# Kernel optimization log

Measured on AMD Instinct MI355X. Metric: run time of the kernel, lower is better.

Reference implementation:

```python
import jax, jax.numpy as jnp
import numpy as np

B, N, S, K = 8, 16384, 1024, 32
C_STEM, C_PATCH, PE_DIM = 64, 128, 24
RADIUS = 0.2
NUM_BANDS = PE_DIM // 6  # 4 freq bands, sin+cos per xyz axis -> 3*2*4 = 24


def setup_inputs() -> dict:
    key = jax.random.key(0)
    ks = jax.random.split(key, 6)
    xyz = jax.random.uniform(ks[0], (B, N, 3), dtype=jnp.float32)
    point_feature = jax.random.normal(ks[1], (B, N, C_STEM), dtype=jnp.float32)
    patch_center = jax.random.uniform(ks[2], (B, S, 3), dtype=jnp.float32)
    in_dim = C_STEM + 3 + PE_DIM  # grouped_feature + relative_xyz + pos-enc
    w1 = jax.random.normal(ks[3], (in_dim, C_PATCH), dtype=jnp.float32) / np.sqrt(in_dim)
    b1 = jnp.zeros((C_PATCH,), dtype=jnp.float32)
    w2 = jax.random.normal(ks[4], (C_PATCH, C_PATCH), dtype=jnp.float32) / np.sqrt(C_PATCH)
    b2 = jnp.zeros((C_PATCH,), dtype=jnp.float32)
    return dict(xyz=xyz, point_feature=point_feature, patch_center=patch_center,
                w1=w1, b1=b1, w2=w2, b2=b2)


def query_ball_point(radius, nsample, xyz, new_xyz):
    # Standard PointNet++ ball query. xyz:[B,N,3], new_xyz:[B,S,3] -> idx:[B,S,K]
    n = xyz.shape[1]
    sqrdists = jnp.sum((new_xyz[:, :, None, :] - xyz[:, None, :, :]) ** 2, axis=-1)  # [B,S,N]
    gi = jnp.where(sqrdists > radius * radius, n,
                   jnp.arange(n, dtype=jnp.int32)[None, None, :])
    gi = jnp.sort(gi, axis=-1)[:, :, :nsample]           # first K in-ball indices
    first = gi[:, :, :1]
    gi = jnp.where(gi == n, first, gi)                   # pad misses with first hit
    return jnp.minimum(gi, n - 1)


def index_points(points, idx):
    # points:[B,N,C], idx:[B,S,K] -> [B,S,K,C]
    b = points.shape[0]
    return points[jnp.arange(b)[:, None, None], idx]


def pos_encode(rel):
    # NeRF-style sinusoidal encoding of relative xyz: [...,3] -> [...,PE_DIM]
    freqs = (2.0 ** jnp.arange(NUM_BANDS, dtype=jnp.float32)) * jnp.pi
    ang = rel[..., None] * freqs                          # [...,3,NB]
    enc = jnp.concatenate([jnp.sin(ang), jnp.cos(ang)], axis=-1)  # [...,3,2NB]
    return enc.reshape(rel.shape[:-1] + (PE_DIM,))


def reference(xyz, point_feature, patch_center, w1, b1, w2, b2):
    neighbor_idx = query_ball_point(RADIUS, K, xyz, patch_center)   # [B,S,K]
    grouped_xyz = index_points(xyz, neighbor_idx)                    # [B,S,K,3]
    grouped_feature = index_points(point_feature, neighbor_idx)      # [B,S,K,C_STEM]
    relative_xyz = grouped_xyz - patch_center[:, :, None, :]
    relative_position = pos_encode(relative_xyz)                     # [B,S,K,PE_DIM]
    grouped_input = jnp.concatenate(
        (grouped_feature, relative_xyz, relative_position), axis=-1)  # [B,S,K,91]
    h = jax.nn.relu(grouped_input @ w1 + b1)   # PointMLP 1 (shared per-point MLP)
    h = h @ w2 + b2                            # PointMLP 2 (no activation)
    patch_feature = jnp.max(h, axis=2)         # max-pool over K neighbors -> [B,S,C_PATCH]
    return (patch_feature, neighbor_idx)
```

## Files before the change

kernel.cpp:

```cpp
#include <hip/hip_runtime.h>
#include <hip/hip_bf16.h>

#define B_ 8
#define N_ 16384
#define S_ 1024
#define K_ 32
#define CSTEM 64
#define CPATCH 128
#define INDIM 91
#define LDH 136

typedef __attribute__((ext_vector_type(8))) short short8v;
typedef __attribute__((ext_vector_type(4))) float f32x4;

static __device__ __forceinline__ unsigned short f2bf(float f) {
  union { float f; unsigned int u; } v; v.f = f;
  return (unsigned short)((v.u + 0x7FFFu + ((v.u >> 16) & 1u)) >> 16);
}

static __device__ __forceinline__ short8v cvt8(const float4 a, const float4 b) {
  unsigned short v[8];
  v[0] = f2bf(a.x); v[1] = f2bf(a.y); v[2] = f2bf(a.z); v[3] = f2bf(a.w);
  v[4] = f2bf(b.x); v[5] = f2bf(b.y); v[6] = f2bf(b.z); v[7] = f2bf(b.w);
  return *(const short8v*)v;
}

static __device__ __forceinline__ short8v pe_frag(
    float r0, float r1, float r2, int kq)
{
  unsigned short v[8];
  #pragma unroll
  for (int j = 0; j < 8; ++j) {
    const int c = 64 + kq + j;
    float val;
    if (c < 67) {
      val = (c == 64) ? r0 : ((c == 65) ? r1 : r2);
    } else if (c < 91) {
      const int qq = c - 67, d = qq >> 3, rbit = qq & 7, band = rbit & 3;
      const float rel = (d == 0) ? r0 : ((d == 1) ? r1 : r2);
      const float ang = rel * ((float)(1 << band) * 3.14159265358979323846f);
      val = (rbit < 4) ? __sinf(ang) : __cosf(ang);
    } else {
      val = 0.f;
    }
    v[j] = f2bf(val);
  }
  return *(const short8v*)v;
}

__global__ __launch_bounds__(256) void pack_weights(
    const float* __restrict__ w1, const float* __restrict__ w2,
    unsigned short* __restrict__ w1p, unsigned short* __restrict__ w2p)
{
  const int id = blockIdx.x * 256 + threadIdx.x;
  if (id < 3 * 8 * 64) {
    const int l = id & 63, ct = (id >> 6) & 7, ks = id >> 9;
    const int col = 16 * ct + (l & 15);
    const int kb = 32 * ks + (l >> 4) * 8;
    unsigned short v[8];
    #pragma unroll
    for (int j = 0; j < 8; ++j) {
      const int k = kb + j;
      v[j] = (k < INDIM) ? f2bf(w1[k * CPATCH + col]) : (unsigned short)0;
    }
    *(short8v*)&w1p[(size_t)id * 8] = *(const short8v*)v;
  } else if (id < 3 * 8 * 64 + 4 * 8 * 64) {
    const int id2 = id - 3 * 8 * 64;
    const int l = id2 & 63, ct = (id2 >> 6) & 7, ks = id2 >> 9;
    const int col = 16 * ct + (l & 15);
    const int kb = 32 * ks + (l >> 4) * 8;
    unsigned short v[8];
    #pragma unroll
    for (int j = 0; j < 8; ++j) v[j] = f2bf(w2[(kb + j) * CPATCH + col]);
    *(short8v*)&w2p[(size_t)id2 * 8] = *(const short8v*)v;
  }
}

#define TEST4(V0, V1, V2, MASKVAR) do {                                    \
    MASKVAR = 0u;                                                          \
    const float X[4] = {(V0).x, (V0).w, (V1).z, (V2).y};                   \
    const float Y[4] = {(V0).y, (V1).x, (V1).w, (V2).z};                   \
    const float Z[4] = {(V0).z, (V1).y, (V2).x, (V2).w};                   \
    _Pragma("unroll")                                                      \
    for (int p = 0; p < 4; ++p) {                                          \
      const float dxf = X[p] - cx, dyf = Y[p] - cy, dzf = Z[p] - cz;       \
      const float d2f = fmaf(dxf, dxf, fmaf(dyf, dyf, dzf * dzf));         \
      bool in;                                                             \
      if (fabsf(d2f - 0.04f) <= 1e-5f) {                                   \
        const double dx = (double)X[p] - (double)cx;                       \
        const double dy = (double)Y[p] - (double)cy;                       \
        const double dz = (double)Z[p] - (double)cz;                       \
        in = (dx * dx + dy * dy + dz * dz) <= (0.2 * 0.2);                 \
      } else {                                                             \
        in = (d2f < 0.04f);                                                \
      }                                                                    \
      if (in) MASKVAR |= (1u << p);                                        \
    }                                                                      \
  } while (0)

#define APPEND4(MASKVAR, POSVAR, I0, V0, V1, V2) do {                      \
    if ((MASKVAR) & 1u) { if ((POSVAR) < K_) { sidx[POSVAR] = (I0) + 0;    \
      sxyz[POSVAR][0] = (V0).x; sxyz[POSVAR][1] = (V0).y;                  \
      sxyz[POSVAR][2] = (V0).z; } ++(POSVAR); }                            \
    if ((MASKVAR) & 2u) { if ((POSVAR) < K_) { sidx[POSVAR] = (I0) + 1;    \
      sxyz[POSVAR][0] = (V0).w; sxyz[POSVAR][1] = (V1).x;                  \
      sxyz[POSVAR][2] = (V1).y; } ++(POSVAR); }                            \
    if ((MASKVAR) & 4u) { if ((POSVAR) < K_) { sidx[POSVAR] = (I0) + 2;    \
      sxyz[POSVAR][0] = (V1).z; sxyz[POSVAR][1] = (V1).w;                  \
      sxyz[POSVAR][2] = (V2).x; } ++(POSVAR); }                            \
    if ((MASKVAR) & 8u) { if ((POSVAR) < K_) { sidx[POSVAR] = (I0) + 3;    \
      sxyz[POSVAR][0] = (V2).y; sxyz[POSVAR][1] = (V2).z;                  \
      sxyz[POSVAR][2] = (V2).w; } ++(POSVAR); }                            \
  } while (0)

__global__ __launch_bounds__(64, 4) void fused_wave(
    const float* __restrict__ xyz, const float* __restrict__ pf,
    const float* __restrict__ pc,
    const unsigned short* __restrict__ w1p, const float* __restrict__ b1,
    const unsigned short* __restrict__ w2p, const float* __restrict__ b2,
    float* __restrict__ idx_out, float* __restrict__ out)
{
  const int lane = threadIdx.x;
  const int bs   = blockIdx.x;
  const int b    = bs >> 10;

  __shared__ int   sidx[K_];
  __shared__ float sxyz[K_][3];
  __shared__ __align__(16) unsigned short Hs[K_][LDH];

  const float* __restrict__ xb  = xyz + (size_t)b * N_ * 3;
  const float* __restrict__ pfb = pf  + (size_t)b * N_ * CSTEM;
  const float cx = pc[bs * 3 + 0];
  const float cy = pc[bs * 3 + 1];
  const float cz = pc[bs * 3 + 2];

  int found = 0;
  {
    const int lo3 = lane * 12;
    int base = 0;
    float4 v0 = *(const float4*)&xb[lo3 + 0];
    float4 v1 = *(const float4*)&xb[lo3 + 4];
    float4 v2 = *(const float4*)&xb[lo3 + 8];
    float4 v3 = *(const float4*)&xb[256 * 3 + lo3 + 0];
    float4 v4 = *(const float4*)&xb[256 * 3 + lo3 + 4];
    float4 v5 = *(const float4*)&xb[256 * 3 + lo3 + 8];

    for (;;) {
      const int nb = (base + 512 < N_) ? base + 512 : base;
      const float4 n0 = *(const float4*)&xb[nb * 3 + lo3 + 0];
      const float4 n1 = *(const float4*)&xb[nb * 3 + lo3 + 4];
      const float4 n2 = *(const float4*)&xb[nb * 3 + lo3 + 8];
      const float4 n3 = *(const float4*)&xb[(nb + 256) * 3 + lo3 + 0];
      const float4 n4 = *(const float4*)&xb[(nb + 256) * 3 + lo3 + 4];
      const float4 n5 = *(const float4*)&xb[(nb + 256) * 3 + lo3 + 8];

      unsigned m0, m1;
      TEST4(v0, v1, v2, m0);
      TEST4(v3, v4, v5, m1);

      const int c0 = __popc(m0), c1 = __popc(m1);
      unsigned incl = (unsigned)c0 | ((unsigned)c1 << 16);
      #pragma unroll
      for (int d = 1; d < 64; d <<= 1) {
        const unsigned t = (unsigned)__shfl_up((int)incl, d);
        if (lane >= d) incl += t;
      }
      const unsigned tot = (unsigned)__shfl((int)incl, 63);
      const int t0 = (int)(tot & 0xFFFFu), t1 = (int)(tot >> 16);

      int pos0 = found + (int)((incl & 0xFFFFu)) - c0;
      int pos1 = found + t0 + (int)(incl >> 16) - c1;
      const int i0 = base + lane * 4;
      APPEND4(m0, pos0, i0, v0, v1, v2);
      APPEND4(m1, pos1, i0 + 256, v3, v4, v5);

      found += t0 + t1;
      if (found >= K_) break;
      base += 512;
      if (base >= N_) break;
      v0 = n0; v1 = n1; v2 = n2; v3 = n3; v4 = n4; v5 = n5;
    }
  }

  if (lane == 0 && found == 0) {
    sidx[0] = N_ - 1;
    sxyz[0][0] = xb[(N_ - 1) * 3 + 0];
    sxyz[0][1] = xb[(N_ - 1) * 3 + 1];
    sxyz[0][2] = xb[(N_ - 1) * 3 + 2];
  }
  __threadfence_block();

  if (lane < K_) {
    const int   fill = sidx[0];
    const float fx = sxyz[0][0];
    const float fy = sxyz[0][1];
    const float fz = sxyz[0][2];
    const int v = (lane < found) ? sidx[lane] : fill;
    if (lane >= found) {
      sidx[lane] = fill;
      sxyz[lane][0] = fx;
      sxyz[lane][1] = fy;
      sxyz[lane][2] = fz;
    }
    idx_out[(size_t)bs * K_ + lane] = (float)v;
  }
  __threadfence_block();

  const int rfr  = lane & 15;
  const int koff = (lane >> 4) * 8;

  const int r0 = sidx[rfr];
  const int r1 = sidx[16 + rfr];
  const float4 u00 = *(const float4*)&pfb[(size_t)r0 * CSTEM + koff];
  const float4 u01 = *(const float4*)&pfb[(size_t)r0 * CSTEM + koff + 4];
  const float4 u02 = *(const float4*)&pfb[(size_t)r0 * CSTEM + 32 + koff];
  const float4 u03 = *(const float4*)&pfb[(size_t)r0 * CSTEM + 32 + koff + 4];
  const float4 u10 = *(const float4*)&pfb[(size_t)r1 * CSTEM + koff];
  const float4 u11 = *(const float4*)&pfb[(size_t)r1 * CSTEM + koff + 4];
  const float4 u12 = *(const float4*)&pfb[(size_t)r1 * CSTEM + 32 + koff];
  const float4 u13 = *(const float4*)&pfb[(size_t)r1 * CSTEM + 32 + koff + 4];

  const short8v a0k2 = pe_frag(sxyz[rfr][0] - cx,
                               sxyz[rfr][1] - cy,
                               sxyz[rfr][2] - cz, koff);
  const short8v a1k2 = pe_frag(sxyz[16 + rfr][0] - cx,
                               sxyz[16 + rfr][1] - cy,
                               sxyz[16 + rfr][2] - cz, koff);
  const short8v a0k0 = cvt8(u00, u01), a0k1 = cvt8(u02, u03);
  const short8v a1k0 = cvt8(u10, u11), a1k1 = cvt8(u12, u13);

  #pragma unroll
  for (int c = 0; c < 4; ++c) {
    const short8v bA0 = *(const short8v*)&w1p[((size_t)(0 * 8 + 2 * c + 0) * 64 + lane) * 8];
    const short8v bA1 = *(const short8v*)&w1p[((size_t)(0 * 8 + 2 * c + 1) * 64 + lane) * 8];
    const short8v bB0 = *(const short8v*)&w1p[((size_t)(1 * 8 + 2 * c + 0) * 64 + lane) * 8];
    const short8v bB1 = *(const short8v*)&w1p[((size_t)(1 * 8 + 2 * c + 1) * 64 + lane) * 8];
    const short8v bC0 = *(const short8v*)&w1p[((size_t)(2 * 8 + 2 * c + 0) * 64 + lane) * 8];
    const short8v bC1 = *(const short8v*)&w1p[((size_t)(2 * 8 + 2 * c + 1) * 64 + lane) * 8];

    f32x4 acc[2][2] = {};
    acc[0][0] = __builtin_amdgcn_mfma_f32_16x16x32_bf16(a0k0, bA0, acc[0][0], 0, 0, 0);
    acc[0][1] = __builtin_amdgcn_mfma_f32_16x16x32_bf16(a0k0, bA1, acc[0][1], 0, 0, 0);
    acc[1][0] = __builtin_amdgcn_mfma_f32_16x16x32_bf16(a1k0, bA0, acc[1][0], 0, 0, 0);
    acc[1][1] = __builtin_amdgcn_mfma_f32_16x16x32_bf16(a1k0, bA1, acc[1][1], 0, 0, 0);
    acc[0][0] = __builtin_amdgcn_mfma_f32_16x16x32_bf16(a0k1, bB0, acc[0][0], 0, 0, 0);
    acc[0][1] = __builtin_amdgcn_mfma_f32_16x16x32_bf16(a0k1, bB1, acc[0][1], 0, 0, 0);
    acc[1][0] = __builtin_amdgcn_mfma_f32_16x16x32_bf16(a1k1, bB0, acc[1][0], 0, 0, 0);
    acc[1][1] = __builtin_amdgcn_mfma_f32_16x16x32_bf16(a1k1, bB1, acc[1][1], 0, 0, 0);
    acc[0][0] = __builtin_amdgcn_mfma_f32_16x16x32_bf16(a0k2, bC0, acc[0][0], 0, 0, 0);
    acc[0][1] = __builtin_amdgcn_mfma_f32_16x16x32_bf16(a0k2, bC1, acc[0][1], 0, 0, 0);
    acc[1][0] = __builtin_amdgcn_mfma_f32_16x16x32_bf16(a1k2, bC0, acc[1][0], 0, 0, 0);
    acc[1][1] = __builtin_amdgcn_mfma_f32_16x16x32_bf16(a1k2, bC1, acc[1][1], 0, 0, 0);

    const float bia0 = b1[32 * c + rfr];
    const float bia1 = b1[32 * c + 16 + rfr];
    #pragma unroll
    for (int rt = 0; rt < 2; ++rt)
      #pragma unroll
      for (int reg = 0; reg < 4; ++reg) {
        const int row = 16 * rt + (lane >> 4) * 4 + reg;
        Hs[row][32 * c + rfr]      = f2bf(fmaxf(acc[rt][0][reg] + bia0, 0.f));
        Hs[row][32 * c + 16 + rfr] = f2bf(fmaxf(acc[rt][1][reg] + bia1, 0.f));
      }
  }

  short8v hf[8];
  #pragma unroll
  for (int ks = 0; ks < 4; ++ks) {
    hf[ks * 2 + 0] = *(const short8v*)&Hs[rfr][ks * 32 + koff];
    hf[ks * 2 + 1] = *(const short8v*)&Hs[16 + rfr][ks * 32 + koff];
  }

  #pragma unroll
  for (int c = 0; c < 4; ++c) {
    f32x4 acc2[2][2] = {};
    #pragma unroll
    for (int ks = 0; ks < 4; ++ks) {
      const short8v b0 = *(const short8v*)&w2p[((size_t)(ks * 8 + 2 * c + 0) * 64 + lane) * 8];
      const short8v b1v = *(const short8v*)&w2p[((size_t)(ks * 8 + 2 * c + 1) * 64 + lane) * 8];
      acc2[0][0] = __builtin_amdgcn_mfma_f32_16x16x32_bf16(hf[ks * 2 + 0], b0,  acc2[0][0], 0, 0, 0);
      acc2[0][1] = __builtin_amdgcn_mfma_f32_16x16x32_bf16(hf[ks * 2 + 0], b1v, acc2[0][1], 0, 0, 0);
      acc2[1][0] = __builtin_amdgcn_mfma_f32_16x16x32_bf16(hf[ks * 2 + 1], b0,  acc2[1][0], 0, 0, 0);
      acc2[1][1] = __builtin_amdgcn_mfma_f32_16x16x32_bf16(hf[ks * 2 + 1], b1v, acc2[1][1], 0, 0, 0);
    }
    float m0 = -3.4e38f, m1 = -3.4e38f;
    #pragma unroll
    for (int rt = 0; rt < 2; ++rt)
      #pragma unroll
      for (int reg = 0; reg < 4; ++reg) {
        m0 = fmaxf(m0, acc2[rt][0][reg]);
        m1 = fmaxf(m1, acc2[rt][1][reg]);
      }
    m0 += b2[32 * c + rfr];
    m1 += b2[32 * c + 16 + rfr];
    m0 = fmaxf(m0, __shfl_xor(m0, 16));
    m0 = fmaxf(m0, __shfl_xor(m0, 32));
    m1 = fmaxf(m1, __shfl_xor(m1, 16));
    m1 = fmaxf(m1, __shfl_xor(m1, 32));
    if (lane < 16) {
      out[(size_t)bs * CPATCH + 32 * c + lane]      = m0;
      out[(size_t)bs * CPATCH + 32 * c + 16 + lane] = m1;
    }
  }
}

extern "C" void kernel_launch(void* const* d_in, const int* in_sizes, int n_in,
                              void* d_out, int out_size, void* d_ws, size_t ws_size,
                              hipStream_t stream) {
  const float* xyz = (const float*)d_in[0];
  const float* pf  = (const float*)d_in[1];
  const float* pc  = (const float*)d_in[2];
  const float* w1  = (const float*)d_in[3];
  const float* b1  = (const float*)d_in[4];
  const float* w2  = (const float*)d_in[5];
  const float* b2  = (const float*)d_in[6];

  float* out     = (float*)d_out;
  float* idx_out = out + (size_t)B_ * S_ * CPATCH;

  unsigned short* w1p = (unsigned short*)d_ws;
  unsigned short* w2p = w1p + 96 * 128;

  pack_weights<<<14, 256, 0, stream>>>(w1, w2, w1p, w2p);
  fused_wave<<<B_ * S_, 64, 0, stream>>>(xyz, pf, pc, w1p, b1, w2p, b2,
                                         idx_out, out);
}
```

Baseline: 46.60 us.

## Process two patch centers per wave to share xyz scans

Each 64-lane block now handles two consecutive patch centers. A single pass over the xyz stream tests every point against both centers, with the two prefix scans packed into one loop, and the MLP stage then runs once per center. The goal is to halve the xyz global reads and the per-block launch overhead by reusing loaded point coordinates. In exchange the scan runs until both centers have K hits, register pressure rises (launch bounds lowered to 3), and the grid shrinks to half as many blocks. An unused w1f preload array was also added and is likely removed by the compiler.

New measurement: 57.18 us. 22.7% more time.

```diff
diff --git a/kernel.cpp b/kernel.cpp
--- a/kernel.cpp
+++ b/kernel.cpp
@@ -76,20 +76,20 @@
   }
 }
 
-#define TEST4(V0, V1, V2, MASKVAR) do {                                    \
+#define TEST4C(V0, V1, V2, CX, CY, CZ, MASKVAR) do {                       \
     MASKVAR = 0u;                                                          \
     const float X[4] = {(V0).x, (V0).w, (V1).z, (V2).y};                   \
     const float Y[4] = {(V0).y, (V1).x, (V1).w, (V2).z};                   \
     const float Z[4] = {(V0).z, (V1).y, (V2).x, (V2).w};                   \
     _Pragma("unroll")                                                      \
     for (int p = 0; p < 4; ++p) {                                          \
-      const float dxf = X[p] - cx, dyf = Y[p] - cy, dzf = Z[p] - cz;       \
+      const float dxf = X[p] - (CX), dyf = Y[p] - (CY), dzf = Z[p] - (CZ); \
       const float d2f = fmaf(dxf, dxf, fmaf(dyf, dyf, dzf * dzf));         \
       bool in;                                                             \
       if (fabsf(d2f - 0.04f) <= 1e-5f) {                                   \
-        const double dx = (double)X[p] - (double)cx;                       \
-        const double dy = (double)Y[p] - (double)cy;                       \
-        const double dz = (double)Z[p] - (double)cz;                       \
+        const double dx = (double)X[p] - (double)(CX);                     \
+        const double dy = (double)Y[p] - (double)(CY);                     \
+        const double dz = (double)Z[p] - (double)(CZ);                     \
         in = (dx * dx + dy * dy + dz * dz) <= (0.2 * 0.2);                 \
       } else {                                                             \
         in = (d2f < 0.04f);                                                \
@@ -98,22 +98,22 @@
     }                                                                      \
   } while (0)
 
-#define APPEND4(MASKVAR, POSVAR, I0, V0, V1, V2) do {                      \
-    if ((MASKVAR) & 1u) { if ((POSVAR) < K_) { sidx[POSVAR] = (I0) + 0;    \
-      sxyz[POSVAR][0] = (V0).x; sxyz[POSVAR][1] = (V0).y;                  \
-      sxyz[POSVAR][2] = (V0).z; } ++(POSVAR); }                            \
-    if ((MASKVAR) & 2u) { if ((POSVAR) < K_) { sidx[POSVAR] = (I0) + 1;    \
-      sxyz[POSVAR][0] = (V0).w; sxyz[POSVAR][1] = (V1).x;                  \
-      sxyz[POSVAR][2] = (V1).y; } ++(POSVAR); }                            \
-    if ((MASKVAR) & 4u) { if ((POSVAR) < K_) { sidx[POSVAR] = (I0) + 2;    \
-      sxyz[POSVAR][0] = (V1).z; sxyz[POSVAR][1] = (V1).w;                  \
-      sxyz[POSVAR][2] = (V2).x; } ++(POSVAR); }                            \
-    if ((MASKVAR) & 8u) { if ((POSVAR) < K_) { sidx[POSVAR] = (I0) + 3;    \
-      sxyz[POSVAR][0] = (V2).y; sxyz[POSVAR][1] = (V2).z;                  \
-      sxyz[POSVAR][2] = (V2).w; } ++(POSVAR); }                            \
+#define APPEND4Q(MASKVAR, POSVAR, I0, V0, V1, V2, Q) do {                  \
+    if ((MASKVAR) & 1u) { if ((POSVAR) < K_) { sidx[Q][POSVAR] = (I0) + 0; \
+      sxyz[Q][POSVAR][0] = (V0).x; sxyz[Q][POSVAR][1] = (V0).y;            \
+      sxyz[Q][POSVAR][2] = (V0).z; } ++(POSVAR); }                         \
+    if ((MASKVAR) & 2u) { if ((POSVAR) < K_) { sidx[Q][POSVAR] = (I0) + 1; \
+      sxyz[Q][POSVAR][0] = (V0).w; sxyz[Q][POSVAR][1] = (V1).x;            \
+      sxyz[Q][POSVAR][2] = (V1).y; } ++(POSVAR); }                         \
+    if ((MASKVAR) & 4u) { if ((POSVAR) < K_) { sidx[Q][POSVAR] = (I0) + 2; \
+      sxyz[Q][POSVAR][0] = (V1).z; sxyz[Q][POSVAR][1] = (V1).w;            \
+      sxyz[Q][POSVAR][2] = (V2).x; } ++(POSVAR); }                         \
+    if ((MASKVAR) & 8u) { if ((POSVAR) < K_) { sidx[Q][POSVAR] = (I0) + 3; \
+      sxyz[Q][POSVAR][0] = (V2).y; sxyz[Q][POSVAR][1] = (V2).z;            \
+      sxyz[Q][POSVAR][2] = (V2).w; } ++(POSVAR); }                         \
   } while (0)
 
-__global__ __launch_bounds__(64, 4) void fused_wave(
+__global__ __launch_bounds__(64, 3) void fused_wave2(
     const float* __restrict__ xyz, const float* __restrict__ pf,
     const float* __restrict__ pc,
     const unsigned short* __restrict__ w1p, const float* __restrict__ b1,
@@ -121,20 +121,19 @@
     float* __restrict__ idx_out, float* __restrict__ out)
 {
   const int lane = threadIdx.x;
-  const int bs   = blockIdx.x;
-  const int b    = bs >> 10;
-
-  __shared__ int   sidx[K_];
-  __shared__ float sxyz[K_][3];
+  const int bs0  = blockIdx.x * 2;
+  const int b    = bs0 >> 10;
+
+  __shared__ int   sidx[2][K_];
+  __shared__ float sxyz[2][K_][3];
   __shared__ __align__(16) unsigned short Hs[K_][LDH];
 
   const float* __restrict__ xb  = xyz + (size_t)b * N_ * 3;
   const float* __restrict__ pfb = pf  + (size_t)b * N_ * CSTEM;
-  const float cx = pc[bs * 3 + 0];
-  const float cy = pc[bs * 3 + 1];
-  const float cz = pc[bs * 3 + 2];
-
-  int found = 0;
+  const float cx0 = pc[bs0 * 3 + 0], cy0 = pc[bs0 * 3 + 1], cz0 = pc[bs0 * 3 + 2];
+  const float cx1 = pc[bs0 * 3 + 3], cy1 = pc[bs0 * 3 + 4], cz1 = pc[bs0 * 3 + 5];
+
+  int found0 = 0, found1 = 0;
   {
     const int lo3 = lane * 12;
     int base = 0;
@@ -154,152 +153,194 @@
       const float4 n4 = *(const float4*)&xb[(nb + 256) * 3 + lo3 + 4];
       const float4 n5 = *(const float4*)&xb[(nb + 256) * 3 + lo3 + 8];
 
-      unsigned m0, m1;
-      TEST4(v0, v1, v2, m0);
-      TEST4(v3, v4, v5, m1);
-
-      const int c0 = __popc(m0), c1 = __popc(m1);
-      unsigned incl = (unsigned)c0 | ((unsigned)c1 << 16);
+      unsigned m00 = 0u, m01 = 0u, m10 = 0u, m11 = 0u;
+      if (found0 < K_) {
+        TEST4C(v0, v1, v2, cx0, cy0, cz0, m00);
+        TEST4C(v3, v4, v5, cx0, cy0, cz0, m10);
+      }
+      if (found1 < K_) {
+        TEST4C(v0, v1, v2, cx1, cy1, cz1, m01);
+        TEST4C(v3, v4, v5, cx1, cy1, cz1, m11);
+      }
+
+      const int c00 = __popc(m00), c01 = __popc(m01);
+      const int c10 = __popc(m10), c11 = __popc(m11);
+      unsigned i0p = (unsigned)c00 | ((unsigned)c01 << 16);
+      unsigned i1p = (unsigned)c10 | ((unsigned)c11 << 16);
       #pragma unroll
       for (int d = 1; d < 64; d <<= 1) {
-        const unsigned t = (unsigned)__shfl_up((int)incl, d);
-        if (lane >= d) incl += t;
-      }
-      const unsigned tot = (unsigned)__shfl((int)incl, 63);
-      const int t0 = (int)(tot & 0xFFFFu), t1 = (int)(tot >> 16);
-
-      int pos0 = found + (int)((incl & 0xFFFFu)) - c0;
-      int pos1 = found + t0 + (int)(incl >> 16) - c1;
+        const unsigned t0 = (unsigned)__shfl_up((int)i0p, d);
+        const unsigned t1 = (unsigned)__shfl_up((int)i1p, d);
+        if (lane >= d) { i0p += t0; i1p += t1; }
+      }
+      const unsigned tot0 = (unsigned)__shfl((int)i0p, 63);
+      const unsigned tot1 = (unsigned)__shfl((int)i1p, 63);
+
       const int i0 = base + lane * 4;
-      APPEND4(m0, pos0, i0, v0, v1, v2);
-      APPEND4(m1, pos1, i0 + 256, v3, v4, v5);
-
-      found += t0 + t1;
-      if (found >= K_) break;
+      int pos00 = found0 + (int)(i0p & 0xFFFFu) - c00;
+      int pos10 = found0 + (int)(tot0 & 0xFFFFu) + (int)(i1p & 0xFFFFu) - c10;
+      int pos01 = found1 + (int)(i0p >> 16) - c01;
+      int pos11 = found1 + (int)(tot0 >> 16) + (int)(i1p >> 16) - c11;
+      APPEND4Q(m00, pos00, i0,       v0, v1, v2, 0);
+      APPEND4Q(m10, pos10, i0 + 256, v3, v4, v5, 0);
+      APPEND4Q(m01, pos01, i0,       v0, v1, v2, 1);
+      APPEND4Q(m11, pos11, i0 + 256, v3, v4, v5, 1);
+
+      found0 += (int)(tot0 & 0xFFFFu) + (int)(tot1 & 0xFFFFu);
+      found1 += (int)(tot0 >> 16) + (int)(tot1 >> 16);
+      if (found0 >= K_ && found1 >= K_) break;
       base += 512;
       if (base >= N_) break;
       v0 = n0; v1 = n1; v2 = n2; v3 = n3; v4 = n4; v5 = n5;
     }
   }
 
-  if (lane == 0 && found == 0) {
-    sidx[0] = N_ - 1;
-    sxyz[0][0] = xb[(N_ - 1) * 3 + 0];
-    sxyz[0][1] = xb[(N_ - 1) * 3 + 1];
-    sxyz[0][2] = xb[(N_ - 1) * 3 + 2];
+  if (lane == 0) {
+    if (found0 == 0) {
+      sidx[0][0] = N_ - 1;
+      sxyz[0][0][0] = xb[(N_ - 1) * 3 + 0];
+      sxyz[0][0][1] = xb[(N_ - 1) * 3 + 1];
+      sxyz[0][0][2] = xb[(N_ - 1) * 3 + 2];
+    }
+    if (found1 == 0) {
+      sidx[1][0] = N_ - 1;
+      sxyz[1][0][0] = xb[(N_ - 1) * 3 + 0];
+      sxyz[1][0][1] = xb[(N_ - 1) * 3 + 1];
+      sxyz[1][0][2] = xb[(N_ - 1) * 3 + 2];
+    }
   }
   __threadfence_block();
 
-  if (lane < K_) {
-    const int   fill = sidx[0];
-    const float fx = sxyz[0][0];
-    const float fy = sxyz[0][1];
-    const float fz = sxyz[0][2];
-    const int v = (lane < found) ? sidx[lane] : fill;
-    if (lane >= found) {
-      sidx[lane] = fill;
-      sxyz[lane][0] = fx;
-      sxyz[lane][1] = fy;
-      sxyz[lane][2] = fz;
-    }
-    idx_out[(size_t)bs * K_ + lane] = (float)v;
+  #pragma unroll
+  for (int q = 0; q < 2; ++q) {
+    const int fnd = q ? found1 : found0;
+    if (lane < K_) {
+      const int   fill = sidx[q][0];
+      const float fx = sxyz[q][0][0];
+      const float fy = sxyz[q][0][1];
+      const float fz = sxyz[q][0][2];
+      const int v = (lane < fnd) ? sidx[q][lane] : fill;
+      if (lane >= fnd) {
+        sidx[q][lane] = fill;
+        sxyz[q][lane][0] = fx;
+        sxyz[q][lane][1] = fy;
+        sxyz[q][lane][2] = fz;
+      }
+      idx_out[(size_t)(bs0 + q) * K_ + lane] = (float)v;
+    }
   }
   __threadfence_block();
 
+  short8v w1f[3][2], w2f[4][2];
+  #pragma unroll
+  for (int ks = 0; ks < 3; ++ks)
+    #pragma unroll
+    for (int t = 0; t < 2; ++t)
+      w1f[ks][t] = *(const short8v*)&w1p[((size_t)(ks * 8 + 0) * 64 + lane) * 8
+                                         + (size_t)(2 * 0 + t) * 0];
   const int rfr  = lane & 15;
   const int koff = (lane >> 4) * 8;
 
-  const int r0 = sidx[rfr];
-  const int r1 = sidx[16 + rfr];
-  const float4 u00 = *(const float4*)&pfb[(size_t)r0 * CSTEM + koff];
-  const float4 u01 = *(const float4*)&pfb[(size_t)r0 * CSTEM + koff + 4];
-  const float4 u02 = *(const float4*)&pfb[(size_t)r0 * CSTEM + 32 + koff];
-  const float4 u03 = *(const float4*)&pfb[(size_t)r0 * CSTEM + 32 + koff + 4];
-  const float4 u10 = *(const float4*)&pfb[(size_t)r1 * CSTEM + koff];
-  const float4 u11 = *(const float4*)&pfb[(size_t)r1 * CSTEM + koff + 4];
-  const float4 u12 = *(const float4*)&pfb[(size_t)r1 * CSTEM + 32 + koff];
-  const float4 u13 = *(const float4*)&pfb[(size_t)r1 * CSTEM + 32 + koff + 4];
-
-  const short8v a0k2 = pe_frag(sxyz[rfr][0] - cx,
-                               sxyz[rfr][1] - cy,
-                               sxyz[rfr][2] - cz, koff);
-  const short8v a1k2 = pe_frag(sxyz[16 + rfr][0] - cx,
-                               sxyz[16 + rfr][1] - cy,
-                               sxyz[16 + rfr][2] - cz, koff);
-  const short8v a0k0 = cvt8(u00, u01), a0k1 = cvt8(u02, u03);
-  const short8v a1k0 = cvt8(u10, u11), a1k1 = cvt8(u12, u13);
-
-  #pragma unroll
-  for (int c = 0; c < 4; ++c) {
-    const short8v bA0 = *(const short8v*)&w1p[((size_t)(0 * 8 + 2 * c + 0) * 64 + lane) * 8];
-    const short8v bA1 = *(const short8v*)&w1p[((size_t)(0 * 8 + 2 * c + 1) * 64 + lane) * 8];
-    const short8v bB0 = *(const short8v*)&w1p[((size_t)(1 * 8 + 2 * c + 0) * 64 + lane) * 8];
-    const short8v bB1 = *(const short8v*)&w1p[((size_t)(1 * 8 + 2 * c + 1) * 64 + lane) * 8];
-    const short8v bC0 = *(const short8v*)&w1p[((size_t)(2 * 8 + 2 * c + 0) * 64 + lane) * 8];
-    const short8v bC1 = *(const short8v*)&w1p[((size_t)(2 * 8 + 2 * c + 1) * 64 + lane) * 8];
-
-    f32x4 acc[2][2] = {};
-    acc[0][0] = __builtin_amdgcn_mfma_f32_16x16x32_bf16(a0k0, bA0, acc[0][0], 0, 0, 0);
-    acc[0][1] = __builtin_amdgcn_mfma_f32_16x16x32_bf16(a0k0, bA1, acc[0][1], 0, 0, 0);
-    acc[1][0] = __builtin_amdgcn_mfma_f32_16x16x32_bf16(a1k0, bA0, acc[1][0], 0, 0, 0);
-    acc[1][1] = __builtin_amdgcn_mfma_f32_16x16x32_bf16(a1k0, bA1, acc[1][1], 0, 0, 0);
-    acc[0][0] = __builtin_amdgcn_mfma_f32_16x16x32_bf16(a0k1, bB0, acc[0][0], 0, 0, 0);
-    acc[0][1] = __builtin_amdgcn_mfma_f32_16x16x32_bf16(a0k1, bB1, acc[0][1], 0, 0, 0);
-    acc[1][0] = __builtin_amdgcn_mfma_f32_16x16x32_bf16(a1k1, bB0, acc[1][0], 0, 0, 0);
-    acc[1][1] = __builtin_amdgcn_mfma_f32_16x16x32_bf16(a1k1, bB1, acc[1][1], 0, 0, 0);
-    acc[0][0] = __builtin_amdgcn_mfma_f32_16x16x32_bf16(a0k2, bC0, acc[0][0], 0, 0, 0);
-    acc[0][1] = __builtin_amdgcn_mfma_f32_16x16x32_bf16(a0k2, bC1, acc[0][1], 0, 0, 0);
-    acc[1][0] = __builtin_amdgcn_mfma_f32_16x16x32_bf16(a1k2, bC0, acc[1][0], 0, 0, 0);
-    acc[1][1] = __builtin_amdgcn_mfma_f32_16x16x32_bf16(a1k2, bC1, acc[1][1], 0, 0, 0);
-
-    const float bia0 = b1[32 * c + rfr];
-    const float bia1 = b1[32 * c + 16 + rfr];
-    #pragma unroll
-    for (int rt = 0; rt < 2; ++rt)
+  {
+    short8v a0k0[2], a0k1[2], a0k2[2], a1k0[2], a1k1[2], a1k2[2];
+    #pragma unroll
+    for (int q = 0; q < 2; ++q) {
+      const float ccx = q ? cx1 : cx0;
+      const float ccy = q ? cy1 : cy0;
+      const float ccz = q ? cz1 : cz0;
+      const int r0 = sidx[q][rfr];
+      const int r1 = sidx[q][16 + rfr];
+      const float4 u00 = *(const float4*)&pfb[(size_t)r0 * CSTEM + koff];
+      const float4 u01 = *(const float4*)&pfb[(size_t)r0 * CSTEM + koff + 4];
+      const float4 u02 = *(const float4*)&pfb[(size_t)r0 * CSTEM + 32 + koff];
+      const float4 u03 = *(const float4*)&pfb[(size_t)r0 * CSTEM + 32 + koff + 4];
+      const float4 u10 = *(const float4*)&pfb[(size_t)r1 * CSTEM + koff];
+      const float4 u11 = *(const float4*)&pfb[(size_t)r1 * CSTEM + koff + 4];
+      const float4 u12 = *(const float4*)&pfb[(size_t)r1 * CSTEM + 32 + koff];
+      const float4 u13 = *(const float4*)&pfb[(size_t)r1 * CSTEM + 32 + koff + 4];
+      a0k0[q] = cvt8(u00, u01); a0k1[q] = cvt8(u02, u03);
+      a1k0[q] = cvt8(u10, u11); a1k1[q] = cvt8(u12, u13);
+      a0k2[q] = pe_frag(sxyz[q][rfr][0] - ccx, sxyz[q][rfr][1] - ccy,
+                        sxyz[q][rfr][2] - ccz, koff);
+      a1k2[q] = pe_frag(sxyz[q][16 + rfr][0] - ccx, sxyz[q][16 + rfr][1] - ccy,
+                        sxyz[q][16 + rfr][2] - ccz, koff);
+    }
+
+    #pragma unroll
+    for (int q = 0; q < 2; ++q) {
       #pragma unroll
-      for (int reg = 0; reg < 4; ++reg) {
-        const int row = 16 * rt + (lane >> 4) * 4 + reg;
-        Hs[row][32 * c + rfr]      = f2bf(fmaxf(acc[rt][0][reg] + bia0, 0.f));
-        Hs[row][32 * c + 16 + rfr] = f2bf(fmaxf(acc[rt][1][reg] + bia1, 0.f));
-      }
-  }
-
-  short8v hf[8];
-  #pragma unroll
-  for (int ks = 0; ks < 4; ++ks) {
-    hf[ks * 2 + 0] = *(const short8v*)&Hs[rfr][ks * 32 + koff];
-    hf[ks * 2 + 1] = *(const short8v*)&Hs[16 + rfr][ks * 32 + koff];
-  }
-
-  #pragma unroll
-  for (int c = 0; c < 4; ++c) {
-    f32x4 acc2[2][2] = {};
-    #pragma unroll
-    for (int ks = 0; ks < 4; ++ks) {
-      const short8v b0 = *(const short8v*)&w2p[((size_t)(ks * 8 + 2 * c + 0) * 64 + lane) * 8];
-      const short8v b1v = *(const short8v*)&w2p[((size_t)(ks * 8 + 2 * c + 1) * 64 + lane) * 8];
-      acc2[0][0] = __builtin_amdgcn_mfma_f32_16x16x32_bf16(hf[ks * 2 + 0], b0,  acc2[0][0], 0, 0, 0);
-      acc2[0][1] = __builtin_amdgcn_mfma_f32_16x16x32_bf16(hf[ks * 2 + 0], b1v, acc2[0][1], 0, 0, 0);
-      acc2[1][0] = __builtin_amdgcn_mfma_f32_16x16x32_bf16(hf[ks * 2 + 1], b0,  acc2[1][0], 0, 0, 0);
-      acc2[1][1] = __builtin_amdgcn_mfma_f32_16x16x32_bf16(hf[ks * 2 + 1], b1v, acc2[1][1], 0, 0, 0);
-    }
-    float m0 = -3.4e38f, m1 = -3.4e38f;
-    #pragma unroll
-    for (int rt = 0; rt < 2; ++rt)
+      for (int c = 0; c < 4; ++c) {
+        const short8v bA0 = *(const short8v*)&w1p[((size_t)(0 * 8 + 2 * c + 0) * 64 + lane) * 8];
+        const short8v bA1 = *(const short8v*)&w1p[((size_t)(0 * 8 + 2 * c + 1) * 64 + lane) * 8];
+        const short8v bB0 = *(const short8v*)&w1p[((size_t)(1 * 8 + 2 * c + 0) * 64 + lane) * 8];
+        const short8v bB1 = *(const short8v*)&w1p[((size_t)(1 * 8 + 2 * c + 1) * 64 + lane) * 8];
+        const short8v bC0 = *(const short8v*)&w1p[((size_t)(2 * 8 + 2 * c + 0) * 64 + lane) * 8];
+        const short8v bC1 = *(const short8v*)&w1p[((size_t)(2 * 8 + 2 * c + 1) * 64 + lane) * 8];
+
+        f32x4 acc[2][2] = {};
+        acc[0][0] = __builtin_amdgcn_mfma_f32_16x16x32_bf16(a0k0[q], bA0, acc[0][0], 0, 0, 0);
+        acc[0][1] = __builtin_amdgcn_mfma_f32_16x16x32_bf16(a0k0[q], bA1, acc[0][1], 0, 0, 0);
+        acc[1][0] = __builtin_amdgcn_mfma_f32_16x16x32_bf16(a1k0[q], bA0, acc[1][0], 0, 0, 0);
+        acc[1][1] = __builtin_amdgcn_mfma_f32_16x16x32_bf16(a1k0[q], bA1, acc[1][1], 0, 0, 0);
+        acc[0][0] = __builtin_amdgcn_mfma_f32_16x16x32_bf16(a0k1[q], bB0, acc[0][0], 0, 0, 0);
+        acc[0][1] = __builtin_amdgcn_mfma_f32_16x16x32_bf16(a0k1[q], bB1, acc[0][1], 0, 0, 0);
+        acc[1][0] = __builtin_amdgcn_mfma_f32_16x16x32_bf16(a1k1[q], bB0, acc[1][0], 0, 0, 0);
+        acc[1][1] = __builtin_amdgcn_mfma_f32_16x16x32_bf16(a1k1[q], bB1, acc[1][1], 0, 0, 0);
+        acc[0][0] = __builtin_amdgcn_mfma_f32_16x16x32_bf16(a0k2[q], bC0, acc[0][0], 0, 0, 0);
+        acc[0][1] = __builtin_amdgcn_mfma_f32_16x16x32_bf16(a0k2[q], bC1, acc[0][1], 0, 0, 0);
+        acc[1][0] = __builtin_amdgcn_mfma_f32_16x16x32_bf16(a1k2[q], bC0, acc[1][0], 0, 0, 0);
+        acc[1][1] = __builtin_amdgcn_mfma_f32_16x16x32_bf16(a1k2[q], bC1, acc[1][1], 0, 0, 0);
+
+        const float bia0 = b1[32 * c + rfr];
+        const float bia1 = b1[32 * c + 16 + rfr];
+        #pragma unroll
+        for (int rt = 0; rt < 2; ++rt)
+          #pragma unroll
+          for (int reg = 0; reg < 4; ++reg) {
+            const int row = 16 * rt + (lane >> 4) * 4 + reg;
+            Hs[row][32 * c + rfr]      = f2bf(fmaxf(acc[rt][0][reg] + bia0, 0.f));
+            Hs[row][32 * c + 16 + rfr] = f2bf(fmaxf(acc[rt][1][reg] + bia1, 0.f));
+          }
+      }
+      short8v hf[8];
       #pragma unroll
-      for (int reg = 0; reg < 4; ++reg) {
-        m0 = fmaxf(m0, acc2[rt][0][reg]);
-        m1 = fmaxf(m1, acc2[rt][1][reg]);
-      }
-    m0 += b2[32 * c + rfr];
-    m1 += b2[32 * c + 16 + rfr];
-    m0 = fmaxf(m0, __shfl_xor(m0, 16));
-    m0 = fmaxf(m0, __shfl_xor(m0, 32));
-    m1 = fmaxf(m1, __shfl_xor(m1, 16));
-    m1 = fmaxf(m1, __shfl_xor(m1, 32));
-    if (lane < 16) {
-      out[(size_t)bs * CPATCH + 32 * c + lane]      = m0;
-      out[(size_t)bs * CPATCH + 32 * c + 16 + lane] = m1;
+      for (int ks = 0; ks < 4; ++ks) {
+        hf[ks * 2 + 0] = *(const short8v*)&Hs[rfr][ks * 32 + koff];
+        hf[ks * 2 + 1] = *(const short8v*)&Hs[16 + rfr][ks * 32 + koff];
+      }
+
+      #pragma unroll
+      for (int c = 0; c < 4; ++c) {
+        f32x4 acc2[2][2] = {};
+        #pragma unroll
+        for (int ks = 0; ks < 4; ++ks) {
+          const short8v b0  = *(const short8v*)&w2p[((size_t)(ks * 8 + 2 * c + 0) * 64 + lane) * 8];
+          const short8v b1v = *(const short8v*)&w2p[((size_t)(ks * 8 + 2 * c + 1) * 64 + lane) * 8];
+          acc2[0][0] = __builtin_amdgcn_mfma_f32_16x16x32_bf16(hf[ks * 2 + 0], b0,  acc2[0][0], 0, 0, 0);
+          acc2[0][1] = __builtin_amdgcn_mfma_f32_16x16x32_bf16(hf[ks * 2 + 0], b1v, acc2[0][1], 0, 0, 0);
+          acc2[1][0] = __builtin_amdgcn_mfma_f32_16x16x32_bf16(hf[ks * 2 + 1], b0,  acc2[1][0], 0, 0, 0);
+          acc2[1][1] = __builtin_amdgcn_mfma_f32_16x16x32_bf16(hf[ks * 2 + 1], b1v, acc2[1][1], 0, 0, 0);
+        }
+        float m0 = -3.4e38f, m1 = -3.4e38f;
+        #pragma unroll
+        for (int rt = 0; rt < 2; ++rt)
+          #pragma unroll
+          for (int reg = 0; reg < 4; ++reg) {
+            m0 = fmaxf(m0, acc2[rt][0][reg]);
+            m1 = fmaxf(m1, acc2[rt][1][reg]);
+          }
+        m0 += b2[32 * c + rfr];
+        m1 += b2[32 * c + 16 + rfr];
+        m0 = fmaxf(m0, __shfl_xor(m0, 16));
+        m0 = fmaxf(m0, __shfl_xor(m0, 32));
+        m1 = fmaxf(m1, __shfl_xor(m1, 16));
+        m1 = fmaxf(m1, __shfl_xor(m1, 32));
+        if (lane < 16) {
+          out[(size_t)(bs0 + q) * CPATCH + 32 * c + lane]      = m0;
+          out[(size_t)(bs0 + q) * CPATCH + 32 * c + 16 + lane] = m1;
+        }
+      }
+      __threadfence_block();
     }
   }
 }
@@ -322,6 +363,6 @@
   unsigned short* w2p = w1p + 96 * 128;
 
   pack_weights<<<14, 256, 0, stream>>>(w1, w2, w1p, w2p);
-  fused_wave<<<B_ * S_, 64, 0, stream>>>(xyz, pf, pc, w1p, b1, w2p, b2,
-                                         idx_out, out);
-}
+  fused_wave2<<<B_ * S_ / 2, 64, 0, stream>>>(xyz, pf, pc, w1p, b1, w2p, b2,
+                                              idx_out, out);
+}
```

## Split ball query and MLP into separate kernels with weight-stationary MLP blocks

Applied to the files above, without the earlier changes.

Splits the fused per-patch wave kernel into a ball-query kernel, which writes indices and gathered xyz to a workspace, and a 256-thread MLP kernel. Each of the MLP kernel's four waves keeps its slice of W1 and W2 in registers across 16 patches. This avoids reloading the weight fragments for every patch and lets the feature gather for the next group of patches overlap with the MFMA work. In exchange it adds a kernel launch, a workspace round-trip for xyz, and several block-wide barriers per patch.

Result: slower. 52.90 us (+13.5%).

```diff
diff --git a/kernel.cpp b/kernel.cpp
--- a/kernel.cpp
+++ b/kernel.cpp
@@ -8,6 +8,7 @@
 #define CSTEM 64
 #define CPATCH 128
 #define INDIM 91
+#define LDA 104
 #define LDH 136
 
 typedef __attribute__((ext_vector_type(8))) short short8v;
@@ -22,29 +23,6 @@
   unsigned short v[8];
   v[0] = f2bf(a.x); v[1] = f2bf(a.y); v[2] = f2bf(a.z); v[3] = f2bf(a.w);
   v[4] = f2bf(b.x); v[5] = f2bf(b.y); v[6] = f2bf(b.z); v[7] = f2bf(b.w);
-  return *(const short8v*)v;
-}
-
-static __device__ __forceinline__ short8v pe_frag(
-    float r0, float r1, float r2, int kq)
-{
-  unsigned short v[8];
-  #pragma unroll
-  for (int j = 0; j < 8; ++j) {
-    const int c = 64 + kq + j;
-    float val;
-    if (c < 67) {
-      val = (c == 64) ? r0 : ((c == 65) ? r1 : r2);
-    } else if (c < 91) {
-      const int qq = c - 67, d = qq >> 3, rbit = qq & 7, band = rbit & 3;
-      const float rel = (d == 0) ? r0 : ((d == 1) ? r1 : r2);
-      const float ang = rel * ((float)(1 << band) * 3.14159265358979323846f);
-      val = (rbit < 4) ? __sinf(ang) : __cosf(ang);
-    } else {
-      val = 0.f;
-    }
-    v[j] = f2bf(val);
-  }
   return *(const short8v*)v;
 }
 
@@ -113,12 +91,9 @@
       sxyz[POSVAR][2] = (V2).w; } ++(POSVAR); }                            \
   } while (0)
 
-__global__ __launch_bounds__(64, 4) void fused_wave(
-    const float* __restrict__ xyz, const float* __restrict__ pf,
-    const float* __restrict__ pc,
-    const unsigned short* __restrict__ w1p, const float* __restrict__ b1,
-    const unsigned short* __restrict__ w2p, const float* __restrict__ b2,
-    float* __restrict__ idx_out, float* __restrict__ out)
+__global__ __launch_bounds__(64, 4) void ball_kernel(
+    const float* __restrict__ xyz, const float* __restrict__ pc,
+    float* __restrict__ idx_out, float* __restrict__ xws)
 {
   const int lane = threadIdx.x;
   const int bs   = blockIdx.x;
@@ -126,10 +101,8 @@
 
   __shared__ int   sidx[K_];
   __shared__ float sxyz[K_][3];
-  __shared__ __align__(16) unsigned short Hs[K_][LDH];
-
-  const float* __restrict__ xb  = xyz + (size_t)b * N_ * 3;
-  const float* __restrict__ pfb = pf  + (size_t)b * N_ * CSTEM;
+
+  const float* __restrict__ xb = xyz + (size_t)b * N_ * 3;
   const float cx = pc[bs * 3 + 0];
   const float cy = pc[bs * 3 + 1];
   const float cz = pc[bs * 3 + 2];
@@ -168,7 +141,7 @@
       const unsigned tot = (unsigned)__shfl((int)incl, 63);
       const int t0 = (int)(tot & 0xFFFFu), t1 = (int)(tot >> 16);
 
-      int pos0 = found + (int)((incl & 0xFFFFu)) - c0;
+      int pos0 = found + (int)(incl & 0xFFFFu) - c0;
       int pos1 = found + t0 + (int)(incl >> 16) - c1;
       const int i0 = base + lane * 4;
       APPEND4(m0, pos0, i0, v0, v1, v2);
@@ -196,110 +169,164 @@
     const float fy = sxyz[0][1];
     const float fz = sxyz[0][2];
     const int v = (lane < found) ? sidx[lane] : fill;
-    if (lane >= found) {
-      sidx[lane] = fill;
-      sxyz[lane][0] = fx;
-      sxyz[lane][1] = fy;
-      sxyz[lane][2] = fz;
-    }
+    const float x = (lane < found) ? sxyz[lane][0] : fx;
+    const float y = (lane < found) ? sxyz[lane][1] : fy;
+    const float z = (lane < found) ? sxyz[lane][2] : fz;
     idx_out[(size_t)bs * K_ + lane] = (float)v;
-  }
-  __threadfence_block();
-
-  const int rfr  = lane & 15;
-  const int koff = (lane >> 4) * 8;
-
-  const int r0 = sidx[rfr];
-  const int r1 = sidx[16 + rfr];
-  const float4 u00 = *(const float4*)&pfb[(size_t)r0 * CSTEM + koff];
-  const float4 u01 = *(const float4*)&pfb[(size_t)r0 * CSTEM + koff + 4];
-  const float4 u02 = *(const float4*)&pfb[(size_t)r0 * CSTEM + 32 + koff];
-  const float4 u03 = *(const float4*)&pfb[(size_t)r0 * CSTEM + 32 + koff + 4];
-  const float4 u10 = *(const float4*)&pfb[(size_t)r1 * CSTEM + koff];
-  const float4 u11 = *(const float4*)&pfb[(size_t)r1 * CSTEM + koff + 4];
-  const float4 u12 = *(const float4*)&pfb[(size_t)r1 * CSTEM + 32 + koff];
-  const float4 u13 = *(const float4*)&pfb[(size_t)r1 * CSTEM + 32 + koff + 4];
-
-  const short8v a0k2 = pe_frag(sxyz[rfr][0] - cx,
-                               sxyz[rfr][1] - cy,
-                               sxyz[rfr][2] - cz, koff);
-  const short8v a1k2 = pe_frag(sxyz[16 + rfr][0] - cx,
-                               sxyz[16 + rfr][1] - cy,
-                               sxyz[16 + rfr][2] - cz, koff);
-  const short8v a0k0 = cvt8(u00, u01), a0k1 = cvt8(u02, u03);
-  const short8v a1k0 = cvt8(u10, u11), a1k1 = cvt8(u12, u13);
-
-  #pragma unroll
-  for (int c = 0; c < 4; ++c) {
-    const short8v bA0 = *(const short8v*)&w1p[((size_t)(0 * 8 + 2 * c + 0) * 64 + lane) * 8];
-    const short8v bA1 = *(const short8v*)&w1p[((size_t)(0 * 8 + 2 * c + 1) * 64 + lane) * 8];
-    const short8v bB0 = *(const short8v*)&w1p[((size_t)(1 * 8 + 2 * c + 0) * 64 + lane) * 8];
-    const short8v bB1 = *(const short8v*)&w1p[((size_t)(1 * 8 + 2 * c + 1) * 64 + lane) * 8];
-    const short8v bC0 = *(const short8v*)&w1p[((size_t)(2 * 8 + 2 * c + 0) * 64 + lane) * 8];
-    const short8v bC1 = *(const short8v*)&w1p[((size_t)(2 * 8 + 2 * c + 1) * 64 + lane) * 8];
-
-    f32x4 acc[2][2] = {};
-    acc[0][0] = __builtin_amdgcn_mfma_f32_16x16x32_bf16(a0k0, bA0, acc[0][0], 0, 0, 0);
-    acc[0][1] = __builtin_amdgcn_mfma_f32_16x16x32_bf16(a0k0, bA1, acc[0][1], 0, 0, 0);
-    acc[1][0] = __builtin_amdgcn_mfma_f32_16x16x32_bf16(a1k0, bA0, acc[1][0], 0, 0, 0);
-    acc[1][1] = __builtin_amdgcn_mfma_f32_16x16x32_bf16(a1k0, bA1, acc[1][1], 0, 0, 0);
-    acc[0][0] = __builtin_amdgcn_mfma_f32_16x16x32_bf16(a0k1, bB0, acc[0][0], 0, 0, 0);
-    acc[0][1] = __builtin_amdgcn_mfma_f32_16x16x32_bf16(a0k1, bB1, acc[0][1], 0, 0, 0);
-    acc[1][0] = __builtin_amdgcn_mfma_f32_16x16x32_bf16(a1k1, bB0, acc[1][0], 0, 0, 0);
-    acc[1][1] = __builtin_amdgcn_mfma_f32_16x16x32_bf16(a1k1, bB1, acc[1][1], 0, 0, 0);
-    acc[0][0] = __builtin_amdgcn_mfma_f32_16x16x32_bf16(a0k2, bC0, acc[0][0], 0, 0, 0);
-    acc[0][1] = __builtin_amdgcn_mfma_f32_16x16x32_bf16(a0k2, bC1, acc[0][1], 0, 0, 0);
-    acc[1][0] = __builtin_amdgcn_mfma_f32_16x16x32_bf16(a1k2, bC0, acc[1][0], 0, 0, 0);
-    acc[1][1] = __builtin_amdgcn_mfma_f32_16x16x32_bf16(a1k2, bC1, acc[1][1], 0, 0, 0);
-
-    const float bia0 = b1[32 * c + rfr];
-    const float bia1 = b1[32 * c + 16 + rfr];
-    #pragma unroll
-    for (int rt = 0; rt < 2; ++rt)
-      #pragma unroll
-      for (int reg = 0; reg < 4; ++reg) {
-        const int row = 16 * rt + (lane >> 4) * 4 + reg;
-        Hs[row][32 * c + rfr]      = f2bf(fmaxf(acc[rt][0][reg] + bia0, 0.f));
-        Hs[row][32 * c + 16 + rfr] = f2bf(fmaxf(acc[rt][1][reg] + bia1, 0.f));
-      }
-  }
-
-  short8v hf[8];
-  #pragma unroll
-  for (int ks = 0; ks < 4; ++ks) {
-    hf[ks * 2 + 0] = *(const short8v*)&Hs[rfr][ks * 32 + koff];
-    hf[ks * 2 + 1] = *(const short8v*)&Hs[16 + rfr][ks * 32 + koff];
-  }
-
-  #pragma unroll
-  for (int c = 0; c < 4; ++c) {
-    f32x4 acc2[2][2] = {};
-    #pragma unroll
-    for (int ks = 0; ks < 4; ++ks) {
-      const short8v b0 = *(const short8v*)&w2p[((size_t)(ks * 8 + 2 * c + 0) * 64 + lane) * 8];
-      const short8v b1v = *(const short8v*)&w2p[((size_t)(ks * 8 + 2 * c + 1) * 64 + lane) * 8];
-      acc2[0][0] = __builtin_amdgcn_mfma_f32_16x16x32_bf16(hf[ks * 2 + 0], b0,  acc2[0][0], 0, 0, 0);
-      acc2[0][1] = __builtin_amdgcn_mfma_f32_16x16x32_bf16(hf[ks * 2 + 0], b1v, acc2[0][1], 0, 0, 0);
-      acc2[1][0] = __builtin_amdgcn_mfma_f32_16x16x32_bf16(hf[ks * 2 + 1], b0,  acc2[1][0], 0, 0, 0);
-      acc2[1][1] = __builtin_amdgcn_mfma_f32_16x16x32_bf16(hf[ks * 2 + 1], b1v, acc2[1][1], 0, 0, 0);
-    }
-    float m0 = -3.4e38f, m1 = -3.4e38f;
-    #pragma unroll
-    for (int rt = 0; rt < 2; ++rt)
-      #pragma unroll
-      for (int reg = 0; reg < 4; ++reg) {
-        m0 = fmaxf(m0, acc2[rt][0][reg]);
-        m1 = fmaxf(m1, acc2[rt][1][reg]);
-      }
-    m0 += b2[32 * c + rfr];
-    m1 += b2[32 * c + 16 + rfr];
-    m0 = fmaxf(m0, __shfl_xor(m0, 16));
-    m0 = fmaxf(m0, __shfl_xor(m0, 32));
-    m1 = fmaxf(m1, __shfl_xor(m1, 16));
-    m1 = fmaxf(m1, __shfl_xor(m1, 32));
-    if (lane < 16) {
-      out[(size_t)bs * CPATCH + 32 * c + lane]      = m0;
-      out[(size_t)bs * CPATCH + 32 * c + 16 + lane] = m1;
+    xws[((size_t)bs * K_ + lane) * 3 + 0] = x;
+    xws[((size_t)bs * K_ + lane) * 3 + 1] = y;
+    xws[((size_t)bs * K_ + lane) * 3 + 2] = z;
+  }
+}
+
+__global__ __launch_bounds__(256, 2) void mlp_persist(
+    const float* __restrict__ pf, const float* __restrict__ pc,
+    const unsigned short* __restrict__ w1p, const float* __restrict__ b1,
+    const unsigned short* __restrict__ w2p, const float* __restrict__ b2,
+    const float* __restrict__ idx_f, const float* __restrict__ xws,
+    float* __restrict__ out)
+{
+  const int tid  = threadIdx.x;
+  const int lane = tid & 63;
+  const int w    = tid >> 6;
+  const int p0   = blockIdx.x * 16;
+  const int b    = p0 >> 10;
+
+  __shared__ __align__(16) unsigned short As[4 * K_][LDA];
+  __shared__ __align__(16) unsigned short Hs[K_][LDH];
+  __shared__ int   sidxAll[16][K_];
+  __shared__ float sxyzAll[16][K_][3];
+  __shared__ float scenAll[16][3];
+
+  const float* __restrict__ pfb = pf + (size_t)b * N_ * CSTEM;
+
+  #pragma unroll
+  for (int t = tid; t < 16 * K_; t += 256)
+    ((int*)sidxAll)[t] = (int)idx_f[(size_t)p0 * K_ + t];
+  #pragma unroll
+  for (int t = tid; t < 16 * K_ * 3; t += 256)
+    ((float*)sxyzAll)[t] = xws[(size_t)p0 * K_ * 3 + t];
+  if (tid < 48) ((float*)scenAll)[tid] = pc[p0 * 3 + tid];
+
+  short8v w1f[3][2], w2f[4][2];
+  #pragma unroll
+  for (int ks = 0; ks < 3; ++ks)
+    #pragma unroll
+    for (int t = 0; t < 2; ++t)
+      w1f[ks][t] = *(const short8v*)&w1p[((size_t)(ks * 8 + 2 * w + t) * 64 + lane) * 8];
+  #pragma unroll
+  for (int ks = 0; ks < 4; ++ks)
+    #pragma unroll
+    for (int t = 0; t < 2; ++t)
+      w2f[ks][t] = *(const short8v*)&w2p[((size_t)(ks * 8 + 2 * w + t) * 64 + lane) * 8];
+  const float bias1[2] = { b1[32 * w + (lane & 15)], b1[32 * w + 16 + (lane & 15)] };
+  const float bias2[2] = { b2[32 * w + (lane & 15)], b2[32 * w + 16 + (lane & 15)] };
+  __syncthreads();
+
+  const int row1 = tid >> 3, sub = tid & 7;
+  const int row2 = tid & 31, j2 = tid >> 5;
+
+  float4 f0a[4], f1a[4];
+  #pragma unroll
+  for (int q = 0; q < 4; ++q) {
+    const int r = sidxAll[q][row1];
+    f0a[q] = *(const float4*)&pfb[(size_t)r * CSTEM + sub * 8];
+    f1a[q] = *(const float4*)&pfb[(size_t)r * CSTEM + sub * 8 + 4];
+  }
+
+  #pragma unroll 1
+  for (int g = 0; g < 4; ++g) {
+    #pragma unroll
+    for (int q = 0; q < 4; ++q)
+      *(short8v*)&As[q * K_ + row1][sub * 8] = cvt8(f0a[q], f1a[q]);
+    #pragma unroll
+    for (int q = 0; q < 4; ++q) {
+      const int p = g * 4 + q;
+      const float r0 = sxyzAll[p][row2][0] - scenAll[p][0];
+      const float r1 = sxyzAll[p][row2][1] - scenAll[p][1];
+      const float r2 = sxyzAll[p][row2][2] - scenAll[p][2];
+      #pragma unroll
+      for (int cc = 0; cc < 4; ++cc) {
+        const int c = 64 + 4 * j2 + cc;
+        float val;
+        if (c < 67) val = (c == 64) ? r0 : ((c == 65) ? r1 : r2);
+        else if (c < 91) {
+          const int qq = c - 67, d = qq >> 3, rbit = qq & 7, band = rbit & 3;
+          const float rel = (d == 0) ? r0 : ((d == 1) ? r1 : r2);
+          const float ang = rel * ((float)(1 << band) * 3.14159265358979323846f);
+          val = (rbit < 4) ? __sinf(ang) : __cosf(ang);
+        } else val = 0.f;
+        As[q * K_ + row2][c] = f2bf(val);
+      }
+    }
+    __syncthreads();
+
+    if (g < 3) {
+      #pragma unroll
+      for (int q = 0; q < 4; ++q) {
+        const int r = sidxAll[(g + 1) * 4 + q][row1];
+        f0a[q] = *(const float4*)&pfb[(size_t)r * CSTEM + sub * 8];
+        f1a[q] = *(const float4*)&pfb[(size_t)r * CSTEM + sub * 8 + 4];
+      }
+    }
+
+    #pragma unroll 1
+    for (int q = 0; q < 4; ++q) {
+      f32x4 acc[2][2] = {};
+      #pragma unroll
+      for (int ks = 0; ks < 3; ++ks) {
+        const int k0 = ks * 32 + (lane >> 4) * 8;
+        const short8v a0 = *(const short8v*)&As[q * K_ + (lane & 15)][k0];
+        const short8v a1 = *(const short8v*)&As[q * K_ + 16 + (lane & 15)][k0];
+        acc[0][0] = __builtin_amdgcn_mfma_f32_16x16x32_bf16(a0, w1f[ks][0], acc[0][0], 0, 0, 0);
+        acc[0][1] = __builtin_amdgcn_mfma_f32_16x16x32_bf16(a0, w1f[ks][1], acc[0][1], 0, 0, 0);
+        acc[1][0] = __builtin_amdgcn_mfma_f32_16x16x32_bf16(a1, w1f[ks][0], acc[1][0], 0, 0, 0);
+        acc[1][1] = __builtin_amdgcn_mfma_f32_16x16x32_bf16(a1, w1f[ks][1], acc[1][1], 0, 0, 0);
+      }
+      #pragma unroll
+      for (int rt = 0; rt < 2; ++rt)
+        #pragma unroll
+        for (int t = 0; t < 2; ++t)
+          #pragma unroll
+          for (int reg = 0; reg < 4; ++reg) {
+            const float h = fmaxf(acc[rt][t][reg] + bias1[t], 0.f);
+            const int row = 16 * rt + (lane >> 4) * 4 + reg;
+            const int col = 32 * w + 16 * t + (lane & 15);
+            Hs[row][col] = f2bf(h);
+          }
+      __syncthreads();
+
+      f32x4 acc2[2][2] = {};
+      #pragma unroll
+      for (int ks = 0; ks < 4; ++ks) {
+        const int k0 = ks * 32 + (lane >> 4) * 8;
+        const short8v a0 = *(const short8v*)&Hs[(lane & 15)][k0];
+        const short8v a1 = *(const short8v*)&Hs[16 + (lane & 15)][k0];
+        acc2[0][0] = __builtin_amdgcn_mfma_f32_16x16x32_bf16(a0, w2f[ks][0], acc2[0][0], 0, 0, 0);
+        acc2[0][1] = __builtin_amdgcn_mfma_f32_16x16x32_bf16(a0, w2f[ks][1], acc2[0][1], 0, 0, 0);
+        acc2[1][0] = __builtin_amdgcn_mfma_f32_16x16x32_bf16(a1, w2f[ks][0], acc2[1][0], 0, 0, 0);
+        acc2[1][1] = __builtin_amdgcn_mfma_f32_16x16x32_bf16(a1, w2f[ks][1], acc2[1][1], 0, 0, 0);
+      }
+      float m0 = -3.4e38f, m1 = -3.4e38f;
+      #pragma unroll
+      for (int rt = 0; rt < 2; ++rt)
+        #pragma unroll
+        for (int reg = 0; reg < 4; ++reg) {
+          m0 = fmaxf(m0, acc2[rt][0][reg]);
+          m1 = fmaxf(m1, acc2[rt][1][reg]);
+        }
+      m0 += bias2[0];
+      m1 += bias2[1];
+      m0 = fmaxf(m0, __shfl_xor(m0, 16));
+      m0 = fmaxf(m0, __shfl_xor(m0, 32));
+      m1 = fmaxf(m1, __shfl_xor(m1, 16));
+      m1 = fmaxf(m1, __shfl_xor(m1, 32));
+      if (lane < 16) {
+        const int bs = p0 + g * 4 + q;
+        out[(size_t)bs * CPATCH + 32 * w + lane]      = m0;
+        out[(size_t)bs * CPATCH + 32 * w + 16 + lane] = m1;
+      }
+      __syncthreads();
     }
   }
 }
@@ -318,10 +345,12 @@
   float* out     = (float*)d_out;
   float* idx_out = out + (size_t)B_ * S_ * CPATCH;
 
-  unsigned short* w1p = (unsigned short*)d_ws;
+  float* xws = (float*)d_ws;
+  unsigned short* w1p = (unsigned short*)(xws + (size_t)B_ * S_ * K_ * 3);
   unsigned short* w2p = w1p + 96 * 128;
 
   pack_weights<<<14, 256, 0, stream>>>(w1, w2, w1p, w2p);
-  fused_wave<<<B_ * S_, 64, 0, stream>>>(xyz, pf, pc, w1p, b1, w2p, b2,
-                                         idx_out, out);
-}
+  ball_kernel<<<B_ * S_, 64, 0, stream>>>(xyz, pc, idx_out, xws);
+  mlp_persist<<<B_ * S_ / 16, 256, 0, stream>>>(pf, pc, w1p, b1, w2p, b2,
+                                                idx_out, xws, out);
+}
```
